# Performance work log

Hardware: AMD Instinct MI355X
Metric: run time of the kernel (lower is better)

## Reference

```python
import math
import jax, jax.numpy as jnp
import numpy as np

D_MODEL = 1024
NUM_HEADS = 16
MAX_SEQ_LEN = 2048
THETA = 10000.0


def setup_inputs() -> dict:
    key = jax.random.key(0)
    ks = jax.random.split(key, 5)
    B, S, D = 2, 2048, D_MODEL
    std = math.sqrt(2.0 / (D + D))
    x = jax.random.normal(ks[0], (B, S, D), dtype=jnp.float32)
    wq = jax.random.normal(ks[1], (D, D), dtype=jnp.float32) * std
    wk = jax.random.normal(ks[2], (D, D), dtype=jnp.float32) * std
    wv = jax.random.normal(ks[3], (D, D), dtype=jnp.float32) * std
    wo = jax.random.normal(ks[4], (D, D), dtype=jnp.float32) * std
    return {"x": x, "wq": wq, "wk": wk, "wv": wv, "wo": wo}


def _rope_tables(seq_len: int, d_k: int):
    # angles[i, k] = i / theta^(2k/d_k), k over d_k//2 pairs
    inv_freq = 1.0 / (THETA ** (jnp.arange(0, d_k, 2, dtype=jnp.float32) / d_k))
    angles = jnp.arange(seq_len, dtype=jnp.float32)[:, None] * inv_freq[None, :]  # [S, d_k/2]
    return jnp.cos(angles), jnp.sin(angles)


def _apply_rope(x, cos, sin):
    # x: [..., S, d_k]; cos/sin: [S, d_k/2], broadcast over leading dims
    x_even = x[..., ::2]
    x_odd = x[..., 1::2]
    r_even = x_even * cos - x_odd * sin
    r_odd = x_even * sin + x_odd * cos
    return jnp.stack([r_even, r_odd], axis=-1).reshape(x.shape)


def reference(x, wq, wk, wv, wo):
    B, S, D = x.shape
    H = NUM_HEADS
    dk = D // H

    def split_heads(t):  # [B,S,D] -> [B,H,S,dk]
        return t.reshape(B, S, H, dk).transpose(0, 2, 1, 3)

    Q = split_heads(x @ wq.T)
    K = split_heads(x @ wk.T)
    V = split_heads(x @ wv.T)

    cos, sin = _rope_tables(S, dk)
    Q = _apply_rope(Q, cos, sin)
    K = _apply_rope(K, cos, sin)

    scores = jnp.einsum('bhqd,bhkd->bhqk', Q, K) / jnp.sqrt(jnp.float32(dk))
    mask = jnp.tril(jnp.ones((S, S), dtype=bool))  # causal: q can attend k <= q
    neg_inf = jnp.float32(-jnp.inf)
    scores = jnp.where(mask, scores, neg_inf)
    m = jnp.max(scores, axis=-1, keepdims=True)
    m = jnp.where(jnp.isinf(m), jnp.zeros_like(m), m)
    exp_scores = jnp.exp(scores - m)
    exp_scores = jnp.where(mask, exp_scores, 0.0)
    attn = exp_scores / (jnp.sum(exp_scores, axis=-1, keepdims=True) + 1e-9)
    out = jnp.einsum('bhqk,bhkd->bhqd', attn, V)  # [B,H,S,dk]
    out = out.transpose(0, 2, 1, 3).reshape(B, S, D)
    return out @ wo.T
```

## Files before the change

### kernel.cpp

```cpp
#include <hip/hip_runtime.h>
#include <stdint.h>

typedef unsigned short u16;
typedef unsigned int u32;
typedef __bf16 bf16x8 __attribute__((ext_vector_type(8)));
typedef float f32x4 __attribute__((ext_vector_type(4)));
typedef unsigned short u16x8 __attribute__((ext_vector_type(8)));

#define D_MODEL 1024
#define SEQ 2048
#define NH 16
#define DK 64
#define NROWS 4096

static __device__ __forceinline__ u16 f2bf(float f) {
  u32 u = __float_as_uint(f);
  u = (u + 0x7FFFu + ((u >> 16) & 1u)) >> 16;
  return (u16)u;
}
static __device__ __forceinline__ float bf2f(u16 h) {
  return __uint_as_float(((u32)h) << 16);
}
static __device__ __forceinline__ f32x4 mfma16(bf16x8 a, bf16x8 b, f32x4 c) {
  return __builtin_amdgcn_mfma_f32_16x16x32_bf16(a, b, c, 0, 0, 0);
}
static __device__ __forceinline__ void gload16(const void* g, void* l) {
  __builtin_amdgcn_global_load_lds(
      (const __attribute__((address_space(1))) void*)g,
      (__attribute__((address_space(3))) void*)l, 16, 0, 0);
}

static __device__ __forceinline__ float xor32_max(float x) {
#if __has_builtin(__builtin_amdgcn_permlane32_swap)
  u32 a = __float_as_uint(x), b = a;
  auto pr = __builtin_amdgcn_permlane32_swap(a, b, false, false);
  return fmaxf(__uint_as_float(pr[0]), __uint_as_float(pr[1]));
#else
  return fmaxf(x, __shfl_xor(x, 32));
#endif
}
static __device__ __forceinline__ float xor32_add(float x) {
#if __has_builtin(__builtin_amdgcn_permlane32_swap)
  u32 a = __float_as_uint(x), b = a;
  auto pr = __builtin_amdgcn_permlane32_swap(a, b, false, false);
  return __uint_as_float(pr[0]) + __uint_as_float(pr[1]);
#else
  return x + __shfl_xor(x, 32);
#endif
}

__global__ __launch_bounds__(256) void k_cast(
    const float* __restrict__ x, const float* __restrict__ wq,
    const float* __restrict__ wk, const float* __restrict__ wv,
    const float* __restrict__ wo, u16* __restrict__ xb, u16* __restrict__ wqb,
    u16* __restrict__ wkb, u16* __restrict__ wvb, u16* __restrict__ wob) {
  size_t e = ((size_t)blockIdx.x * 256 + threadIdx.x) * 8;
  const float* s;
  u16* d;
  size_t off;
  if (e < (size_t)NROWS * D_MODEL) {
    s = x; d = xb; off = e;
  } else {
    size_t r = e - (size_t)NROWS * D_MODEL;
    unsigned wi = (unsigned)(r >> 20);
    off = r & 1048575u;
    s = wi == 0 ? wq : wi == 1 ? wk : wi == 2 ? wv : wo;
    d = wi == 0 ? wqb : wi == 1 ? wkb : wi == 2 ? wvb : wob;
  }
  float4 a = *(const float4*)(s + off);
  float4 b = *(const float4*)(s + off + 4);
  u16x8 o;
  o[0] = f2bf(a.x); o[1] = f2bf(a.y); o[2] = f2bf(a.z); o[3] = f2bf(a.w);
  o[4] = f2bf(b.x); o[5] = f2bf(b.y); o[6] = f2bf(b.z); o[7] = f2bf(b.w);
  *(u16x8*)(d + off) = o;
}

__global__ __launch_bounds__(256) void k_tab(float2* __restrict__ cs) {
  int i = blockIdx.x * 256 + threadIdx.x;
  int s = i >> 5, p = i & 31;
  double ang = (double)s * pow(10000.0, -(double)p / 32.0);
  cs[i] = make_float2((float)cos(ang), (float)sin(ang));
}

__global__ __launch_bounds__(256, 1) void k_gemmqkv(
    const u16* __restrict__ A, const u16* __restrict__ B0,
    const u16* __restrict__ B1, const u16* __restrict__ B2,
    const float2* __restrict__ cs, u16* __restrict__ qh,
    u16* __restrict__ kh, u16* __restrict__ vt) {
  constexpr int K = 1024;
  const int mb = blockIdx.x, nb = blockIdx.y;
  const int tid = threadIdx.x;
  const int lane = tid & 63, w = tid >> 6;
  const int lq = lane & 15, lg = lane >> 4;
  const int wm = w >> 1, wn = w & 1;
  __shared__ __align__(16) u16 As[128 * 32];
  __shared__ __align__(16) u16 Bs[128 * 32];
  __shared__ __align__(16) u16 Tr[128][136];

  const int sel = nb >> 3;
  const u16* Bp = sel == 0 ? B0 : (sel == 1 ? B1 : B2);
  const int nloc = (nb & 7) * 128;
  const char* Ab = (const char*)A + (size_t)mb * 128 * 2048;
  const char* Bb = (const char*)Bp + (size_t)nloc * 2048;

  const int srow = tid >> 2;
  const int scb = (tid & 3) * 16;

  f32x4 zero4 = {0.f, 0.f, 0.f, 0.f};
  f32x4 acc[4][4];
#pragma unroll
  for (int i = 0; i < 4; ++i)
#pragma unroll
    for (int j = 0; j < 4; ++j) acc[i][j] = zero4;

  for (int k0 = 0; k0 < K; k0 += 32) {
#pragma unroll
    for (int c = 0; c < 2; ++c) {
      int o = c * 4096 + tid * 16;
      const char* ga = Ab + (size_t)(c * 64 + srow) * 2048 + k0 * 2 + scb;
      const char* gb = Bb + (size_t)(c * 64 + srow) * 2048 + k0 * 2 + scb;
      gload16(ga, (char*)As + o);
      gload16(gb, (char*)Bs + o);
    }
    __syncthreads();
    bf16x8 af[4], bfr[4];
#pragma unroll
    for (int i = 0; i < 4; ++i) {
      af[i] = *(const bf16x8*)((const char*)As + (wm * 64 + i * 16 + lq) * 64 + lg * 16);
      bfr[i] = *(const bf16x8*)((const char*)Bs + (wn * 64 + i * 16 + lq) * 64 + lg * 16);
    }
#pragma unroll
    for (int i = 0; i < 4; ++i)
#pragma unroll
      for (int j = 0; j < 4; ++j) acc[i][j] = mfma16(af[i], bfr[j], acc[i][j]);
    __syncthreads();
  }

  if (sel < 2) {
    u16* dst = sel ? kh : qh;
    const float qs = sel ? 1.0f : 0.18033688011112042f;
    const bool oddl = (lane & 1) != 0;
#pragma unroll
    for (int i = 0; i < 4; ++i) {
#pragma unroll
      for (int r = 0; r < 4; ++r) {
        int rowg = mb * 128 + wm * 64 + i * 16 + lg * 4 + r;
        int s = rowg & 2047, b = rowg >> 11;
        const float2* csrow = cs + s * 32;
#pragma unroll
        for (int j = 0; j < 4; ++j) {
          int colL = nloc + wn * 64 + j * 16 + lq;
          float v = acc[i][j][r];
          float pv = __shfl_xor(v, 1);
          float2 c2 = csrow[(colL & 63) >> 1];
          float t = pv * c2.y;
          float res = (v * c2.x + (oddl ? t : -t)) * qs;
          int h = colL >> 6, d = colL & 63;
          dst[((size_t)(b * 16 + h) * 2048 + s) * 64 + d] = f2bf(res);
        }
      }
    }
  } else {
#pragma unroll
    for (int i = 0; i < 4; ++i)
#pragma unroll
      for (int j = 0; j < 4; ++j)
#pragma unroll
        for (int r = 0; r < 4; ++r) {
          int cb = wn * 64 + j * 16 + lq;
          int rb = wm * 64 + i * 16 + lg * 4 + r;
          Tr[cb][rb] = f2bf(acc[i][j][r]);
        }
    __syncthreads();
    const int b = mb >> 4;
    const int s0 = (mb & 15) * 128 + (tid & 1) * 64;
    const int d128 = tid >> 1;
    const int h = (nb & 7) * 2 + (d128 >> 6);
    const int d = d128 & 63;
    u16* vrow = vt + ((size_t)(b * 16 + h) * 64 + d) * 2048 + s0;
    const u16* trow = &Tr[d128][(tid & 1) * 64];
#pragma unroll
    for (int c = 0; c < 8; ++c)
      *(u16x8*)(vrow + c * 8) = *(const u16x8*)(trow + c * 8);
  }
}

__global__ __launch_bounds__(256, 1) void k_gemm(
    const u16* __restrict__ A, const u16* __restrict__ B0,
    float* __restrict__ Cf, int ldc) {
  constexpr int K = 1024;
  const int mb = blockIdx.x, nb = blockIdx.y;
  const int tid = threadIdx.x;
  const int lane = tid & 63, w = tid >> 6;
  const int lq = lane & 15, lg = lane >> 4;
  const int wm = w >> 1, wn = w & 1;
  __shared__ __align__(16) u16 As[128 * 32];
  __shared__ __align__(16) u16 Bs[128 * 32];

  const char* Ab = (const char*)A + (size_t)mb * 128 * 2048;
  const char* Bb = (const char*)B0 + (size_t)(nb * 128) * 2048;

  const int srow = tid >> 2;
  const int scb = (tid & 3) * 16;

  f32x4 zero4 = {0.f, 0.f, 0.f, 0.f};
  f32x4 acc[4][4];
#pragma unroll
  for (int i = 0; i < 4; ++i)
#pragma unroll
    for (int j = 0; j < 4; ++j) acc[i][j] = zero4;

  for (int k0 = 0; k0 < K; k0 += 32) {
#pragma unroll
    for (int c = 0; c < 2; ++c) {
      int o = c * 4096 + tid * 16;
      const char* ga = Ab + (size_t)(c * 64 + srow) * 2048 + k0 * 2 + scb;
      const char* gb = Bb + (size_t)(c * 64 + srow) * 2048 + k0 * 2 + scb;
      gload16(ga, (char*)As + o);
      gload16(gb, (char*)Bs + o);
    }
    __syncthreads();
    bf16x8 af[4], bfr[4];
#pragma unroll
    for (int i = 0; i < 4; ++i) {
      af[i] = *(const bf16x8*)((const char*)As + (wm * 64 + i * 16 + lq) * 64 + lg * 16);
      bfr[i] = *(const bf16x8*)((const char*)Bs + (wn * 64 + i * 16 + lq) * 64 + lg * 16);
    }
#pragma unroll
    for (int i = 0; i < 4; ++i)
#pragma unroll
      for (int j = 0; j < 4; ++j) acc[i][j] = mfma16(af[i], bfr[j], acc[i][j]);
    __syncthreads();
  }

#pragma unroll
  for (int i = 0; i < 4; ++i) {
#pragma unroll
    for (int r = 0; r < 4; ++r) {
      size_t rowg = (size_t)(mb * 128 + wm * 64 + i * 16 + lg * 4 + r);
#pragma unroll
      for (int j = 0; j < 4; ++j) {
        int colg = nb * 128 + wn * 64 + j * 16 + lq;
        Cf[rowg * ldc + colg] = acc[i][j][r];
      }
    }
  }
}

static __device__ __forceinline__ void attn_tile(
    const u16* Kl, const u16* Vl, u16* Plw, int k0, int qrow, int lq, int lg,
    bf16x8 qf0, bf16x8 qf1, float& m_run, float& l_run, f32x4* accO, bool masked) {
  f32x4 zero4 = {0.f, 0.f, 0.f, 0.f};
  f32x4 sa[4];
  sa[0] = zero4; sa[1] = zero4; sa[2] = zero4; sa[3] = zero4;
  __builtin_amdgcn_s_setprio(1);
#pragma unroll
  for (int kt = 0; kt < 4; ++kt) {
    int krow = kt * 16 + lq;
    int base = krow * 128 + lg * 16;
    int swz = (krow & 7) << 4;
    bf16x8 kf0 = *(const bf16x8*)((const char*)Kl + (base ^ swz));
    bf16x8 kf1 = *(const bf16x8*)((const char*)Kl + ((base + 64) ^ swz));
    sa[kt] = mfma16(kf0, qf0, sa[kt]);
    sa[kt] = mfma16(kf1, qf1, sa[kt]);
  }
  __builtin_amdgcn_s_setprio(0);

  float p[16];
#pragma unroll
  for (int kt = 0; kt < 4; ++kt)
#pragma unroll
    for (int r = 0; r < 4; ++r) p[kt * 4 + r] = sa[kt][r];
  if (masked) {
#pragma unroll
    for (int kt = 0; kt < 4; ++kt)
#pragma unroll
      for (int r = 0; r < 4; ++r) {
        int key = k0 + kt * 16 + lg * 4 + r;
        if (key > qrow) p[kt * 4 + r] = -1e30f;
      }
  }
  float x0 = fmaxf(p[0], p[1]), x1 = fmaxf(p[2], p[3]);
  float x2 = fmaxf(p[4], p[5]), x3 = fmaxf(p[6], p[7]);
  float x4 = fmaxf(p[8], p[9]), x5 = fmaxf(p[10], p[11]);
  float x6 = fmaxf(p[12], p[13]), x7 = fmaxf(p[14], p[15]);
  x0 = fmaxf(x0, x1); x2 = fmaxf(x2, x3); x4 = fmaxf(x4, x5); x6 = fmaxf(x6, x7);
  x0 = fmaxf(x0, x2); x4 = fmaxf(x4, x6);
  float pm = fmaxf(x0, x4);
  pm = fmaxf(pm, __shfl_xor(pm, 16));
  pm = xor32_max(pm);
  const bool resc = __any(pm > m_run + 8.0f);
  float mnew = resc ? fmaxf(m_run, pm) : m_run;
#pragma unroll
  for (int i = 0; i < 16; ++i) p[i] = __builtin_amdgcn_exp2f(p[i] - mnew);
  float s0 = p[0] + p[1], s1 = p[2] + p[3], s2 = p[4] + p[5], s3 = p[6] + p[7];
  float s4 = p[8] + p[9], s5 = p[10] + p[11], s6 = p[12] + p[13], s7 = p[14] + p[15];
  s0 += s1; s2 += s3; s4 += s5; s6 += s7;
  s0 += s2; s4 += s6;
  float rs = s0 + s4;
  rs += __shfl_xor(rs, 16);
  rs = xor32_add(rs);
  if (resc) {
    float alpha = __builtin_amdgcn_exp2f(m_run - mnew);
    l_run = l_run * alpha + rs;
    m_run = mnew;
#pragma unroll
    for (int r = 0; r < 4; ++r) {
      float ar = __shfl(alpha, lg * 4 + r);
#pragma unroll
      for (int dt = 0; dt < 4; ++dt) accO[dt][r] *= ar;
    }
  } else {
    l_run += rs;
  }

  {
    int swz = (lq & 7) << 4;
#pragma unroll
    for (int kt = 0; kt < 4; ++kt) {
      u32 w0, w1;
      asm("v_cvt_pk_bf16_f32 %0, %1, %2"
          : "=v"(w0) : "v"(p[kt * 4 + 0]), "v"(p[kt * 4 + 1]));
      asm("v_cvt_pk_bf16_f32 %0, %1, %2"
          : "=v"(w1) : "v"(p[kt * 4 + 2]), "v"(p[kt * 4 + 3]));
      int a0 = (lq * 128 + (kt * 16 + lg * 4) * 2) ^ swz;
      int a1 = (lq * 128 + (kt * 16 + lg * 4 + 2) * 2) ^ swz;
      *(u32*)((char*)Plw + a0) = w0;
      *(u32*)((char*)Plw + a1) = w1;
    }
  }
  {
    int swz = (lq & 7) << 4;
    bf16x8 pa0 = *(const bf16x8*)((const char*)Plw + ((lq * 128 + lg * 16) ^ swz));
    bf16x8 pa1 = *(const bf16x8*)((const char*)Plw + ((lq * 128 + 64 + lg * 16) ^ swz));
    __builtin_amdgcn_s_setprio(1);
#pragma unroll
    for (int dt = 0; dt < 4; ++dt) {
      int vrow = dt * 16 + lq;
      int vb = vrow * 128 + lg * 16;
      int vs = (vrow & 7) << 4;
      bf16x8 v0 = *(const bf16x8*)((const char*)Vl + (vb ^ vs));
      bf16x8 v1 = *(const bf16x8*)((const char*)Vl + ((vb + 64) ^ vs));
      accO[dt] = mfma16(pa0, v0, accO[dt]);
      accO[dt] = mfma16(pa1, v1, accO[dt]);
    }
    __builtin_amdgcn_s_setprio(0);
  }
}

__global__ __launch_bounds__(256, 2) void k_attn(const u16* __restrict__ qh,
                                                 const u16* __restrict__ kh,
                                                 const u16* __restrict__ vt,
                                                 u16* __restrict__ ao) {
  const int qb1 = (int)blockIdx.x;
  const int qb2 = 31 - qb1;
  const int bh = blockIdx.y;
  const int tid = threadIdx.x;
  const int w = tid >> 6;
  const int lane = tid & 63;
  const int lq = lane & 15;
  const int lg = lane >> 4;

  __shared__ __align__(16) u16 Kd[2][2][64 * 64];
  __shared__ __align__(16) u16 Vd[2][2][64 * 64];
  __shared__ __align__(16) u16 Pl[4][16 * 64];

  const int qtop1 = qb1 * 64 + w * 16;
  const int qtop2 = qb2 * 64 + w * 16;
  const int qrow1 = qtop1 + lq;
  const int qrow2 = qtop2 + lq;

  const u16* qp1 = qh + ((size_t)bh * SEQ + qrow1) * DK + lg * 8;
  const u16* qp2 = qh + ((size_t)bh * SEQ + qrow2) * DK + lg * 8;
  bf16x8 qa0 = *(const bf16x8*)qp1;
  bf16x8 qa1 = *(const bf16x8*)(qp1 + 32);
  bf16x8 qc0 = *(const bf16x8*)qp2;
  bf16x8 qc1 = *(const bf16x8*)(qp2 + 32);

  f32x4 zero4 = {0.f, 0.f, 0.f, 0.f};
  f32x4 acc1[4], acc2[4];
#pragma unroll
  for (int dt = 0; dt < 4; ++dt) { acc1[dt] = zero4; acc2[dt] = zero4; }
  float m1 = -1e30f, l1 = 0.f, m2 = -1e30f, l2 = 0.f;

  const int nt1 = qb1 + 1;
  const int nt2 = qb2 + 1;
  const int NIT = (nt2 + 1) >> 1;

  const char* kb_ = (const char*)kh + (size_t)bh * SEQ * 128;
  const char* vb_ = (const char*)vt + (size_t)bh * DK * 4096;

#pragma unroll
  for (int s = 0; s < 2; ++s)
#pragma unroll
    for (int pass = 0; pass < 2; ++pass) {
      int chunk = pass * 256 + tid;
      int srow = chunk >> 3;
      int colb = ((chunk & 7) * 16) ^ ((srow & 7) << 4);
      gload16(kb_ + (size_t)(s * 64 + srow) * 128 + colb,
              (char*)Kd[0][s] + chunk * 16);
      gload16(vb_ + (size_t)srow * 4096 + (s * 64) * 2 + colb,
              (char*)Vd[0][s] + chunk * 16);
    }
  __syncthreads();

  for (int it = 0; it < NIT; ++it) {
    const int cur = it & 1;
    if (it + 1 < NIT) {
      int kb0 = (it + 1) * 128;
#pragma unroll
      for (int s = 0; s < 2; ++s)
#pragma unroll
        for (int pass = 0; pass < 2; ++pass) {
          int chunk = pass * 256 + tid;
          int srow = chunk >> 3;
          int colb = ((chunk & 7) * 16) ^ ((srow & 7) << 4);
          gload16(kb_ + (size_t)(kb0 + s * 64 + srow) * 128 + colb,
                  (char*)Kd[cur ^ 1][s] + chunk * 16);
          gload16(vb_ + (size_t)srow * 4096 + (kb0 + s * 64) * 2 + colb,
                  (char*)Vd[cur ^ 1][s] + chunk * 16);
        }
    }
#pragma unroll
    for (int s = 0; s < 2; ++s) {
      const int tsub = it * 2 + s;
      const int k0 = tsub * 64;
      if (tsub < nt1)
        attn_tile(Kd[cur][s], Vd[cur][s], Pl[w], k0, qrow1, lq, lg, qa0, qa1,
                  m1, l1, acc1, tsub == nt1 - 1);
      if (tsub < nt2)
        attn_tile(Kd[cur][s], Vd[cur][s], Pl[w], k0, qrow2, lq, lg, qc0, qc1,
                  m2, l2, acc2, tsub == nt2 - 1);
    }
    __syncthreads();
  }

  const int b = bh >> 4, h = bh & 15;
#pragma unroll
  for (int r = 0; r < 4; ++r) {
    float lr = __shfl(l1, lg * 4 + r);
    float inv = 1.f / (lr + 1e-9f);
    int qq = qtop1 + lg * 4 + r;
    u16* orow = ao + ((size_t)b * SEQ + qq) * D_MODEL + h * DK;
#pragma unroll
    for (int dt = 0; dt < 4; ++dt) orow[dt * 16 + lq] = f2bf(acc1[dt][r] * inv);
  }
#pragma unroll
  for (int r = 0; r < 4; ++r) {
    float lr = __shfl(l2, lg * 4 + r);
    float inv = 1.f / (lr + 1e-9f);
    int qq = qtop2 + lg * 4 + r;
    u16* orow = ao + ((size_t)b * SEQ + qq) * D_MODEL + h * DK;
#pragma unroll
    for (int dt = 0; dt < 4; ++dt) orow[dt * 16 + lq] = f2bf(acc2[dt][r] * inv);
  }
}

extern "C" void kernel_launch(void* const* d_in, const int* in_sizes, int n_in,
                              void* d_out, int out_size, void* d_ws, size_t ws_size,
                              hipStream_t stream) {
  const float* x = (const float*)d_in[0];
  const float* wq = (const float*)d_in[1];
  const float* wk = (const float*)d_in[2];
  const float* wv = (const float*)d_in[3];
  const float* wo = (const float*)d_in[4];
  float* out = (float*)d_out;
  char* ws = (char*)d_ws;

  u16* xb    = (u16*)(ws + 0);
  u16* wqb   = (u16*)(ws + 8388608);
  u16* wkb   = (u16*)(ws + 10485760);
  u16* wvb   = (u16*)(ws + 12582912);
  u16* wob   = (u16*)(ws + 14680064);
  u16* qhb   = (u16*)(ws + 41943040);
  u16* khb   = (u16*)(ws + 50331648);
  u16* vtb   = (u16*)(ws + 58720256);
  u16* aob   = (u16*)(ws + 67108864);
  float2* cs = (float2*)(ws + 75497472);

  k_cast<<<4096, 256, 0, stream>>>(x, wq, wk, wv, wo, xb, wqb, wkb, wvb, wob);
  k_tab<<<256, 256, 0, stream>>>(cs);
  k_gemmqkv<<<dim3(32, 24), 256, 0, stream>>>(xb, wqb, wkb, wvb, cs, qhb, khb, vtb);
  k_attn<<<dim3(16, 32), 256, 0, stream>>>(qhb, khb, vtb, aob);
  k_gemm<<<dim3(32, 8), 256, 0, stream>>>(aob, wob, out, 1024);
}
```

Baseline: 131.8 us.

## Split V transpose into separate kernel and halve output GEMM tile width

```diff
diff --git a/kernel.cpp b/kernel.cpp
--- a/kernel.cpp
+++ b/kernel.cpp
@@ -86,7 +86,7 @@
     const u16* __restrict__ A, const u16* __restrict__ B0,
     const u16* __restrict__ B1, const u16* __restrict__ B2,
     const float2* __restrict__ cs, u16* __restrict__ qh,
-    u16* __restrict__ kh, u16* __restrict__ vt) {
+    u16* __restrict__ kh, u16* __restrict__ vtmp) {
   constexpr int K = 1024;
   const int mb = blockIdx.x, nb = blockIdx.y;
   const int tid = threadIdx.x;
@@ -95,7 +95,6 @@
   const int wm = w >> 1, wn = w & 1;
   __shared__ __align__(16) u16 As[128 * 32];
   __shared__ __align__(16) u16 Bs[128 * 32];
-  __shared__ __align__(16) u16 Tr[128][136];
 
   const int sel = nb >> 3;
   const u16* Bp = sel == 0 ? B0 : (sel == 1 ? B1 : B2);
@@ -162,32 +161,48 @@
     }
   } else {
 #pragma unroll
-    for (int i = 0; i < 4; ++i)
-#pragma unroll
-      for (int j = 0; j < 4; ++j)
-#pragma unroll
-        for (int r = 0; r < 4; ++r) {
-          int cb = wn * 64 + j * 16 + lq;
-          int rb = wm * 64 + i * 16 + lg * 4 + r;
-          Tr[cb][rb] = f2bf(acc[i][j][r]);
+    for (int i = 0; i < 4; ++i) {
+#pragma unroll
+      for (int r = 0; r < 4; ++r) {
+        size_t rowg = (size_t)(mb * 128 + wm * 64 + i * 16 + lg * 4 + r);
+#pragma unroll
+        for (int j = 0; j < 4; ++j) {
+          int colg = nloc + wn * 64 + j * 16 + lq;
+          vtmp[rowg * 1024 + colg] = f2bf(acc[i][j][r]);
         }
-    __syncthreads();
-    const int b = mb >> 4;
-    const int s0 = (mb & 15) * 128 + (tid & 1) * 64;
-    const int d128 = tid >> 1;
-    const int h = (nb & 7) * 2 + (d128 >> 6);
-    const int d = d128 & 63;
-    u16* vrow = vt + ((size_t)(b * 16 + h) * 64 + d) * 2048 + s0;
-    const u16* trow = &Tr[d128][(tid & 1) * 64];
-#pragma unroll
-    for (int c = 0; c < 8; ++c)
-      *(u16x8*)(vrow + c * 8) = *(const u16x8*)(trow + c * 8);
-  }
-}
-
-__global__ __launch_bounds__(256, 1) void k_gemm(
-    const u16* __restrict__ A, const u16* __restrict__ B0,
-    float* __restrict__ Cf, int ldc) {
+      }
+    }
+  }
+}
+
+__global__ __launch_bounds__(256) void k_vtrans(const u16* __restrict__ vtmp,
+                                                u16* __restrict__ vt) {
+  __shared__ __align__(16) u16 t[64][72];
+  int sb = blockIdx.x, bh = blockIdx.y;
+  int b = bh >> 4, h = bh & 15;
+  int tid = threadIdx.x;
+#pragma unroll
+  for (int c = 0; c < 2; ++c) {
+    int o = tid * 8 + c * 2048;
+    int r = o >> 6, d = o & 63;
+    u16x8 v = *(const u16x8*)(vtmp + (size_t)(b * SEQ + sb * 64 + r) * 1024 + h * 64 + d);
+    *(u16x8*)&t[r][d] = v;
+  }
+  __syncthreads();
+#pragma unroll
+  for (int c = 0; c < 2; ++c) {
+    int o = tid * 8 + c * 2048;
+    int d = o >> 6, si = o & 63;
+    u16x8 v;
+#pragma unroll
+    for (int j = 0; j < 8; ++j) v[j] = t[si + j][d];
+    *(u16x8*)(vt + ((size_t)bh * 64 + d) * SEQ + sb * 64 + si) = v;
+  }
+}
+
+__global__ __launch_bounds__(256, 2) void k_gemmo(const u16* __restrict__ A,
+                                                  const u16* __restrict__ B0,
+                                                  float* __restrict__ Cf) {
   constexpr int K = 1024;
   const int mb = blockIdx.x, nb = blockIdx.y;
   const int tid = threadIdx.x;
@@ -195,41 +210,40 @@
   const int lq = lane & 15, lg = lane >> 4;
   const int wm = w >> 1, wn = w & 1;
   __shared__ __align__(16) u16 As[128 * 32];
-  __shared__ __align__(16) u16 Bs[128 * 32];
+  __shared__ __align__(16) u16 Bs[64 * 32];
 
   const char* Ab = (const char*)A + (size_t)mb * 128 * 2048;
-  const char* Bb = (const char*)B0 + (size_t)(nb * 128) * 2048;
+  const char* Bb = (const char*)B0 + (size_t)(nb * 64) * 2048;
 
   const int srow = tid >> 2;
   const int scb = (tid & 3) * 16;
 
   f32x4 zero4 = {0.f, 0.f, 0.f, 0.f};
-  f32x4 acc[4][4];
-#pragma unroll
-  for (int i = 0; i < 4; ++i)
-#pragma unroll
-    for (int j = 0; j < 4; ++j) acc[i][j] = zero4;
+  f32x4 acc[4][2];
+#pragma unroll
+  for (int i = 0; i < 4; ++i) {
+    acc[i][0] = zero4; acc[i][1] = zero4;
+  }
 
   for (int k0 = 0; k0 < K; k0 += 32) {
 #pragma unroll
     for (int c = 0; c < 2; ++c) {
-      int o = c * 4096 + tid * 16;
       const char* ga = Ab + (size_t)(c * 64 + srow) * 2048 + k0 * 2 + scb;
-      const char* gb = Bb + (size_t)(c * 64 + srow) * 2048 + k0 * 2 + scb;
-      gload16(ga, (char*)As + o);
-      gload16(gb, (char*)Bs + o);
-    }
+      gload16(ga, (char*)As + c * 4096 + tid * 16);
+    }
+    gload16(Bb + (size_t)srow * 2048 + k0 * 2 + scb, (char*)Bs + tid * 16);
     __syncthreads();
-    bf16x8 af[4], bfr[4];
-#pragma unroll
-    for (int i = 0; i < 4; ++i) {
+    bf16x8 af[4], bfr[2];
+#pragma unroll
+    for (int i = 0; i < 4; ++i)
       af[i] = *(const bf16x8*)((const char*)As + (wm * 64 + i * 16 + lq) * 64 + lg * 16);
-      bfr[i] = *(const bf16x8*)((const char*)Bs + (wn * 64 + i * 16 + lq) * 64 + lg * 16);
-    }
+#pragma unroll
+    for (int j = 0; j < 2; ++j)
+      bfr[j] = *(const bf16x8*)((const char*)Bs + (wn * 32 + j * 16 + lq) * 64 + lg * 16);
 #pragma unroll
     for (int i = 0; i < 4; ++i)
 #pragma unroll
-      for (int j = 0; j < 4; ++j) acc[i][j] = mfma16(af[i], bfr[j], acc[i][j]);
+      for (int j = 0; j < 2; ++j) acc[i][j] = mfma16(af[i], bfr[j], acc[i][j]);
     __syncthreads();
   }
 
@@ -239,9 +253,9 @@
     for (int r = 0; r < 4; ++r) {
       size_t rowg = (size_t)(mb * 128 + wm * 64 + i * 16 + lg * 4 + r);
 #pragma unroll
-      for (int j = 0; j < 4; ++j) {
-        int colg = nb * 128 + wn * 64 + j * 16 + lq;
-        Cf[rowg * ldc + colg] = acc[i][j][r];
+      for (int j = 0; j < 2; ++j) {
+        int colg = nb * 64 + wn * 32 + j * 16 + lq;
+        Cf[rowg * 1024 + colg] = acc[i][j][r];
       }
     }
   }
@@ -472,6 +486,7 @@
   u16* wkb   = (u16*)(ws + 10485760);
   u16* wvb   = (u16*)(ws + 12582912);
   u16* wob   = (u16*)(ws + 14680064);
+  u16* vtmp  = (u16*)(ws + 16777216);
   u16* qhb   = (u16*)(ws + 41943040);
   u16* khb   = (u16*)(ws + 50331648);
   u16* vtb   = (u16*)(ws + 58720256);
@@ -480,7 +495,8 @@
 
   k_cast<<<4096, 256, 0, stream>>>(x, wq, wk, wv, wo, xb, wqb, wkb, wvb, wob);
   k_tab<<<256, 256, 0, stream>>>(cs);
-  k_gemmqkv<<<dim3(32, 24), 256, 0, stream>>>(xb, wqb, wkb, wvb, cs, qhb, khb, vtb);
+  k_gemmqkv<<<dim3(32, 24), 256, 0, stream>>>(xb, wqb, wkb, wvb, cs, qhb, khb, vtmp);
+  k_vtrans<<<dim3(32, 32), 256, 0, stream>>>(vtmp, vtb);
   k_attn<<<dim3(16, 32), 256, 0, stream>>>(qhb, khb, vtb, aob);
-  k_gemm<<<dim3(32, 8), 256, 0, stream>>>(aob, wob, out, 1024);
-}
+  k_gemmo<<<dim3(32, 16), 256, 0, stream>>>(aob, wob, out);
+}
```

Result: no change. 129.3 us (-1.9%).
